# Performance work log

Measured on AMD Instinct MI355X. Metric: run time of the kernel, lower is better.

Reference implementation:

```python
import jax, jax.numpy as jnp
import numpy as np

EPS = 1e-06  # used both as eps and as the F.threshold threshold (mqjs passes eps as th)


def _pair_log_dist_sum(x1, x2, th):
    # dist[i,j] = ||x1_i||^2 + ||x2_j||^2 - 2 x1_i . x2_j  (n x n)
    x1x2 = x1 @ x2.T
    sq1 = jnp.sum(x1 * x1, axis=1)[:, None]
    sq2 = jnp.sum(x2 * x2, axis=1)[None, :]
    dist = sq1 + sq2 - 2.0 * x1x2
    # F.threshold(dist, th, 1): values <= th -> 1; then clamp(min=1), sqrt, log, row-sum
    dist = jnp.where(dist > th, dist, 1.0)
    dist = jnp.maximum(dist, 1.0)
    return jnp.sum(0.5 * jnp.log(dist), axis=1)  # log(sqrt(d)) == 0.5*log(d)


def _mqjs(inp, tgt, eps):
    n = inp.shape[0]
    x1 = inp.reshape(n, -1)
    x2 = tgt.reshape(n, -1)
    p = (x1 + x2) / 2.0
    ce = _pair_log_dist_sum(x1, p, eps) + _pair_log_dist_sum(x2, p, eps)
    se = _pair_log_dist_sum(x1, x1, eps) * (n / (n - 1))
    return jnp.mean(ce - se)


def setup_inputs() -> dict:
    key = jax.random.key(0)
    k1, k2 = jax.random.split(key)
    n, d = 8192, 256
    inp = jax.random.normal(k1, (n, d), dtype=jnp.float32)
    tgt = jax.random.normal(k2, (n, d), dtype=jnp.float32)
    return {"input": inp, "target": tgt}


def reference(input, target):
    return _mqjs(input, target, EPS)
```

## Files before the change

### kernel.cpp

```cpp
#include <hip/hip_runtime.h>

#define N 8192
#define D 256
#define BM 128
#define BJ 64
#define JG 8
#define GJ (N / BJ / JG)
#define GI (N / BM)

typedef int   i32x4 __attribute__((ext_vector_type(4)));
typedef int   i32x8 __attribute__((ext_vector_type(8)));
typedef float f32x4 __attribute__((ext_vector_type(4)));
typedef float f32x2 __attribute__((ext_vector_type(2)));

__device__ __forceinline__ unsigned pack_fp8x4(float a, float b, float c, float d) {
    unsigned lo = __builtin_amdgcn_cvt_pk_fp8_f32(a, b, 0, false);
    return __builtin_amdgcn_cvt_pk_fp8_f32(c, d, lo, true);
}
__device__ __forceinline__ float dequant_sumsq(unsigned q) {
    const float v0 = __builtin_amdgcn_cvt_f32_fp8(q, 0);
    const float v1 = __builtin_amdgcn_cvt_f32_fp8(q, 1);
    const float v2 = __builtin_amdgcn_cvt_f32_fp8(q, 2);
    const float v3 = __builtin_amdgcn_cvt_f32_fp8(q, 3);
    return fmaf(v0, v0, fmaf(v1, v1, fmaf(v2, v2, v3 * v3)));
}

__global__ void prep_kernel(const float* __restrict__ x1, const float* __restrict__ x2,
                            unsigned* __restrict__ x1q, unsigned* __restrict__ x2q,
                            unsigned* __restrict__ pq,
                            float* __restrict__ sq1, float* __restrict__ sq2,
                            float* __restrict__ sqp) {
    const int tid = threadIdx.x, lane = tid & 63, wv = tid >> 6;
    const int row = blockIdx.x * 4 + wv;
    const size_t eb = (size_t)row * D + lane * 4;
    const float4 a = *(const float4*)(x1 + eb);
    const float4 b = *(const float4*)(x2 + eb);
    const float px = 0.5f * (a.x + b.x), py = 0.5f * (a.y + b.y);
    const float pz = 0.5f * (a.z + b.z), pw = 0.5f * (a.w + b.w);
    const unsigned qa = pack_fp8x4(a.x, a.y, a.z, a.w);
    const unsigned qb = pack_fp8x4(b.x, b.y, b.z, b.w);
    const unsigned qp = pack_fp8x4(px, py, pz, pw);
    const size_t wb = (size_t)row * (D / 4) + lane;
    x1q[wb] = qa; x2q[wb] = qb; pq[wb] = qp;
    float s1 = dequant_sumsq(qa), s2 = dequant_sumsq(qb), sp = dequant_sumsq(qp);
    #pragma unroll
    for (int o = 32; o > 0; o >>= 1) {
        s1 += __shfl_down(s1, o, 64);
        s2 += __shfl_down(s2, o, 64);
        sp += __shfl_down(sp, o, 64);
    }
    if (lane == 0) { sq1[row] = s1; sq2[row] = s2; sqp[row] = sp; }
}

__device__ __forceinline__ f32x4 mfma8(i32x8 a, i32x8 b, f32x4 c) {
    return __builtin_amdgcn_mfma_scale_f32_16x16x128_f8f6f4(
        a, b, c, 0, 0, 0, 0x7F7F7F7F, 0, 0x7F7F7F7F);
}

__device__ __forceinline__ i32x8 read_frag(const unsigned char* Ts, int m, int quad) {
    const int r7 = m & 7;
    const i32x4 lo = *(const i32x4*)(Ts + m * 128 + ((((2 * quad)     ^ r7)) << 4));
    const i32x4 hi = *(const i32x4*)(Ts + m * 128 + ((((2 * quad + 1) ^ r7)) << 4));
    i32x8 f;
    f[0] = lo[0]; f[1] = lo[1]; f[2] = lo[2]; f[3] = lo[3];
    f[4] = hi[0]; f[5] = hi[1]; f[6] = hi[2]; f[7] = hi[3];
    return f;
}

__device__ __forceinline__ void stageA(const unsigned char* __restrict__ g,
                                       unsigned char* s, int rowbase, size_t kb,
                                       int wv, int srow, int sblk) {
    #pragma unroll
    for (int it = 0; it < 4; ++it) {
        const int grp = wv * 4 + it;
        const int row = grp * 8 + srow;
        __builtin_amdgcn_global_load_lds(
            (const __attribute__((address_space(1))) void*)(g + (size_t)(rowbase + row) * D + kb + sblk * 16),
            (__attribute__((address_space(3))) void*)(s + grp * 1024), 16, 0, 0);
    }
}
__device__ __forceinline__ void stageB(const unsigned char* __restrict__ g,
                                       unsigned char* s, int rowbase, size_t kb,
                                       int wv, int srow, int sblk) {
    #pragma unroll
    for (int it = 0; it < 2; ++it) {
        const int grp = wv * 2 + it;
        const int row = grp * 8 + srow;
        __builtin_amdgcn_global_load_lds(
            (const __attribute__((address_space(1))) void*)(g + (size_t)(rowbase + row) * D + kb + sblk * 16),
            (__attribute__((address_space(3))) void*)(s + grp * 1024), 16, 0, 0);
    }
}

__device__ __forceinline__ float logsumP(const f32x4 (&acc)[4][2],
                                         const float* __restrict__ sqA,
                                         const float sb[2], int wr, int quad) {
    float s = 0.0f;
    #pragma unroll
    for (int ti = 0; ti < 4; ++ti) {
        const int base = wr * 64 + ti * 16 + quad * 4;
        const f32x2 sa01 = {sqA[base], sqA[base + 1]};
        const f32x2 sa23 = {sqA[base + 2], sqA[base + 3]};
        f32x2 pr = {1.0f, 1.0f};
        #pragma unroll
        for (int tj = 0; tj < 2; ++tj) {
            const f32x2 sbv = {sb[tj], sb[tj]};
            const f32x2 t01 = sa01 + sbv, t23 = sa23 + sbv;
            const f32x2 v01 = {acc[ti][tj][0], acc[ti][tj][1]};
            const f32x2 v23 = {acc[ti][tj][2], acc[ti][tj][3]};
            f32x2 d01 = t01 - 2.0f * v01;
            f32x2 d23 = t23 - 2.0f * v23;
            d01 = __builtin_elementwise_max(d01, (f32x2){1.0f, 1.0f});
            d23 = __builtin_elementwise_max(d23, (f32x2){1.0f, 1.0f});
            pr *= d01; pr *= d23;
        }
        s += __logf(pr.x * pr.y);
    }
    return s;
}

__device__ __forceinline__ float logsumStraddle(const f32x4 (&acc)[4][2],
                                                const float* __restrict__ sqA,
                                                const float sb[2],
                                                int wr, int wc, int quad, int l15,
                                                int I0, int J0) {
    float s = 0.0f;
    #pragma unroll
    for (int ti = 0; ti < 4; ++ti) {
        #pragma unroll
        for (int tj = 0; tj < 2; ++tj) {
            const int j = J0 + wc * 32 + tj * 16 + l15;
            float pr = 1.0f;
            #pragma unroll
            for (int r = 0; r < 4; ++r) {
                const int i = I0 + wr * 64 + ti * 16 + quad * 4 + r;
                float d = fmaf(-2.0f, acc[ti][tj][r],
                               sqA[wr * 64 + ti * 16 + quad * 4 + r] + sb[tj]);
                d = fmaxf(d, 1.0f);
                const float t = (j > i) ? d : 1.0f;
                const float u = (j >= i) ? d : 1.0f;
                pr *= t * u;
            }
            s += __logf(pr);
        }
    }
    return s;
}

__global__ __launch_bounds__(256) void mqjs_main(
    const unsigned char* __restrict__ x1q, const unsigned char* __restrict__ x2q,
    const unsigned char* __restrict__ pq,
    const float* __restrict__ sq1, const float* __restrict__ sq2,
    const float* __restrict__ sqp, float* __restrict__ partials) {

    __shared__ __align__(16) unsigned char A2s[2 * BM * 128];
    __shared__ __align__(16) unsigned char BAs[2 * BJ * 128];
    __shared__ __align__(16) unsigned char BBs[2 * BJ * 128];
    __shared__ float sqa1[BM], sqa2[BM];
    __shared__ float red[4];

    const int tid = threadIdx.x;
    const int lane = tid & 63;
    const int wv = tid >> 6;
    const int wr = wv >> 1, wc = wv & 1;
    const int quad = lane >> 4, l15 = lane & 15;

    const int I0 = blockIdx.y * BM;
    const int jbase = blockIdx.x * JG;
    const float wse = -(float)N / (float)(N - 1);

    const int srow = lane >> 3;
    const int sblk = (lane & 7) ^ srow;

    stageA(x1q, A2s,         I0, 0,   wv, srow, sblk);
    stageA(x1q, A2s + 16384, I0, 128, wv, srow, sblk);
    stageB(pq,  BAs,         jbase * BJ, 0,   wv, srow, sblk);
    stageB(pq,  BAs + 8192,  jbase * BJ, 128, wv, srow, sblk);
    if (tid < BM) sqa1[tid] = sq1[I0 + tid];
    else          sqa2[tid - BM] = sq2[I0 + tid - BM];
    __syncthreads();

    i32x8 a1f[2][4];
    #pragma unroll
    for (int kc = 0; kc < 2; ++kc)
        #pragma unroll
        for (int ti = 0; ti < 4; ++ti)
            a1f[kc][ti] = read_frag(A2s + kc * 16384, wr * 64 + ti * 16 + l15, quad);
    __syncthreads();
    stageA(x2q, A2s,         I0, 0,   wv, srow, sblk);
    stageA(x2q, A2s + 16384, I0, 128, wv, srow, sblk);
    __syncthreads();

    float tsum = 0.0f;

    for (int jj = 0; jj < JG; ++jj) {
        const int J0 = (jbase + jj) * BJ;
        const bool doSym = (J0 >= I0);
        const bool full  = (J0 >= I0 + BM);

        f32x4 acc0[4][2], acc1[4][2];
        #pragma unroll
        for (int a = 0; a < 4; ++a)
            #pragma unroll
            for (int b = 0; b < 2; ++b) {
                acc0[a][b] = (f32x4){0.f, 0.f, 0.f, 0.f};
                acc1[a][b] = (f32x4){0.f, 0.f, 0.f, 0.f};
            }
        #pragma unroll
        for (int kc = 0; kc < 2; ++kc) {
            i32x8 bfr[2];
            #pragma unroll
            for (int tj = 0; tj < 2; ++tj)
                bfr[tj] = read_frag(BAs + kc * 8192, wc * 32 + tj * 16 + l15, quad);
            #pragma unroll
            for (int ti = 0; ti < 4; ++ti) {
                const i32x8 a2 = read_frag(A2s + kc * 16384, wr * 64 + ti * 16 + l15, quad);
                #pragma unroll
                for (int tj = 0; tj < 2; ++tj) {
                    acc0[ti][tj] = mfma8(a1f[kc][ti], bfr[tj], acc0[ti][tj]);
                    acc1[ti][tj] = mfma8(a2,          bfr[tj], acc1[ti][tj]);
                }
            }
        }

        if (doSym) {
            stageB(x1q, BBs,        J0, 0,   wv, srow, sblk);
            stageB(x1q, BBs + 8192, J0, 128, wv, srow, sblk);
        }

        {
            float sbp[2];
            #pragma unroll
            for (int tj = 0; tj < 2; ++tj) sbp[tj] = sqp[J0 + wc * 32 + tj * 16 + l15];
            tsum += 0.5f * logsumP(acc0, sqa1, sbp, wr, quad);
            tsum += 0.5f * logsumP(acc1, sqa2, sbp, wr, quad);
        }
        __syncthreads();

        f32x4 acc2[4][2];
        if (doSym) {
            #pragma unroll
            for (int a = 0; a < 4; ++a)
                #pragma unroll
                for (int b = 0; b < 2; ++b)
                    acc2[a][b] = (f32x4){0.f, 0.f, 0.f, 0.f};
            #pragma unroll
            for (int kc = 0; kc < 2; ++kc) {
                i32x8 bfr[2];
                #pragma unroll
                for (int tj = 0; tj < 2; ++tj)
                    bfr[tj] = read_frag(BBs + kc * 8192, wc * 32 + tj * 16 + l15, quad);
                #pragma unroll
                for (int ti = 0; ti < 4; ++ti)
                    #pragma unroll
                    for (int tj = 0; tj < 2; ++tj)
                        acc2[ti][tj] = mfma8(a1f[kc][ti], bfr[tj], acc2[ti][tj]);
            }
        }

        if (jj < JG - 1) {
            stageB(pq, BAs,        (jbase + jj + 1) * BJ, 0,   wv, srow, sblk);
            stageB(pq, BAs + 8192, (jbase + jj + 1) * BJ, 128, wv, srow, sblk);
        }

        if (doSym) {
            float sbx[2];
            #pragma unroll
            for (int tj = 0; tj < 2; ++tj) sbx[tj] = sq1[J0 + wc * 32 + tj * 16 + l15];
            if (full)
                tsum += wse * logsumP(acc2, sqa1, sbx, wr, quad);
            else
                tsum += 0.5f * wse * logsumStraddle(acc2, sqa1, sbx, wr, wc, quad, l15, I0, J0);
        }
        __syncthreads();
    }

    #pragma unroll
    for (int o = 32; o > 0; o >>= 1) tsum += __shfl_down(tsum, o, 64);
    if (lane == 0) red[wv] = tsum;
    __syncthreads();
    if (tid == 0)
        partials[blockIdx.y * GJ + blockIdx.x] = red[0] + red[1] + red[2] + red[3];
}

__global__ void finalize_kernel(const float* __restrict__ partials, float* __restrict__ out) {
    const int tid = threadIdx.x;
    const float4 v = ((const float4*)partials)[tid];
    double s = (double)v.x + (double)v.y + (double)v.z + (double)v.w;
    #pragma unroll
    for (int o = 32; o > 0; o >>= 1) s += __shfl_down(s, o, 64);
    __shared__ double r[4];
    if ((tid & 63) == 0) r[tid >> 6] = s;
    __syncthreads();
    if (tid == 0) out[0] = (float)((r[0] + r[1] + r[2] + r[3]) / (double)N);
}

extern "C" void kernel_launch(void* const* d_in, const int* in_sizes, int n_in,
                              void* d_out, int out_size, void* d_ws, size_t ws_size,
                              hipStream_t stream) {
    const float* x1 = (const float*)d_in[0];
    const float* x2 = (const float*)d_in[1];

    char* ws = (char*)d_ws;
    const size_t MBYTES = (size_t)N * D;
    unsigned* x1q = (unsigned*)(ws);
    unsigned* x2q = (unsigned*)(ws + MBYTES);
    unsigned* pq  = (unsigned*)(ws + 2 * MBYTES);
    float* sq1 = (float*)(ws + 3 * MBYTES);
    float* sq2 = (float*)(ws + 3 * MBYTES + (size_t)N * 4);
    float* sqp = (float*)(ws + 3 * MBYTES + (size_t)N * 8);
    float* partials = (float*)(ws + 3 * MBYTES + (size_t)N * 12);

    prep_kernel<<<N / 4, 256, 0, stream>>>(x1, x2, x1q, x2q, pq, sq1, sq2, sqp);
    mqjs_main<<<dim3(GJ, GI), 256, 0, stream>>>(
        (const unsigned char*)x1q, (const unsigned char*)x2q, (const unsigned char*)pq,
        sq1, sq2, sqp, partials);
    finalize_kernel<<<1, 256, 0, stream>>>(partials, (float*)d_out);
}
```

Measured before the change: 153.5 us.

## Merge B buffers, halve j-group, fuse finalize via atomic last-block reduction

Measured after the change: 186.4 us. 21.5% more time.

```diff
diff --git a/kernel.cpp b/kernel.cpp
--- a/kernel.cpp
+++ b/kernel.cpp
@@ -4,9 +4,10 @@
 #define D 256
 #define BM 128
 #define BJ 64
-#define JG 8
+#define JG 4
 #define GJ (N / BJ / JG)
 #define GI (N / BM)
+#define NBLK (GJ * GI)
 
 typedef int   i32x4 __attribute__((ext_vector_type(4)));
 typedef int   i32x8 __attribute__((ext_vector_type(8)));
@@ -29,9 +30,11 @@
                             unsigned* __restrict__ x1q, unsigned* __restrict__ x2q,
                             unsigned* __restrict__ pq,
                             float* __restrict__ sq1, float* __restrict__ sq2,
-                            float* __restrict__ sqp) {
+                            float* __restrict__ sqp, double* __restrict__ acc,
+                            unsigned* __restrict__ ctr) {
     const int tid = threadIdx.x, lane = tid & 63, wv = tid >> 6;
     const int row = blockIdx.x * 4 + wv;
+    if (blockIdx.x == 0 && tid == 0) { *acc = 0.0; *ctr = 0u; }
     const size_t eb = (size_t)row * D + lane * 4;
     const float4 a = *(const float4*)(x1 + eb);
     const float4 b = *(const float4*)(x2 + eb);
@@ -151,11 +154,11 @@
     const unsigned char* __restrict__ x1q, const unsigned char* __restrict__ x2q,
     const unsigned char* __restrict__ pq,
     const float* __restrict__ sq1, const float* __restrict__ sq2,
-    const float* __restrict__ sqp, float* __restrict__ partials) {
+    const float* __restrict__ sqp, double* __restrict__ acc_out,
+    unsigned* __restrict__ ctr, float* __restrict__ out) {
 
     __shared__ __align__(16) unsigned char A2s[2 * BM * 128];
-    __shared__ __align__(16) unsigned char BAs[2 * BJ * 128];
-    __shared__ __align__(16) unsigned char BBs[2 * BJ * 128];
+    __shared__ __align__(16) unsigned char Bs [2 * BJ * 128];
     __shared__ float sqa1[BM], sqa2[BM];
     __shared__ float red[4];
 
@@ -174,8 +177,8 @@
 
     stageA(x1q, A2s,         I0, 0,   wv, srow, sblk);
     stageA(x1q, A2s + 16384, I0, 128, wv, srow, sblk);
-    stageB(pq,  BAs,         jbase * BJ, 0,   wv, srow, sblk);
-    stageB(pq,  BAs + 8192,  jbase * BJ, 128, wv, srow, sblk);
+    stageB(pq,  Bs,          jbase * BJ, 0,   wv, srow, sblk);
+    stageB(pq,  Bs + 8192,   jbase * BJ, 128, wv, srow, sblk);
     if (tid < BM) sqa1[tid] = sq1[I0 + tid];
     else          sqa2[tid - BM] = sq2[I0 + tid - BM];
     __syncthreads();
@@ -198,7 +201,7 @@
         const bool doSym = (J0 >= I0);
         const bool full  = (J0 >= I0 + BM);
 
-        f32x4 acc0[4][2], acc1[4][2];
+        f32x4 acc0[4][2], acc1[4][2], acc2[4][2];
         #pragma unroll
         for (int a = 0; a < 4; ++a)
             #pragma unroll
@@ -211,7 +214,7 @@
             i32x8 bfr[2];
             #pragma unroll
             for (int tj = 0; tj < 2; ++tj)
-                bfr[tj] = read_frag(BAs + kc * 8192, wc * 32 + tj * 16 + l15, quad);
+                bfr[tj] = read_frag(Bs + kc * 8192, wc * 32 + tj * 16 + l15, quad);
             #pragma unroll
             for (int ti = 0; ti < 4; ++ti) {
                 const i32x8 a2 = read_frag(A2s + kc * 16384, wr * 64 + ti * 16 + l15, quad);
@@ -222,12 +225,12 @@
                 }
             }
         }
+        __syncthreads();
 
         if (doSym) {
-            stageB(x1q, BBs,        J0, 0,   wv, srow, sblk);
-            stageB(x1q, BBs + 8192, J0, 128, wv, srow, sblk);
-        }
-
+            stageB(x1q, Bs,        J0, 0,   wv, srow, sblk);
+            stageB(x1q, Bs + 8192, J0, 128, wv, srow, sblk);
+        }
         {
             float sbp[2];
             #pragma unroll
@@ -235,10 +238,9 @@
             tsum += 0.5f * logsumP(acc0, sqa1, sbp, wr, quad);
             tsum += 0.5f * logsumP(acc1, sqa2, sbp, wr, quad);
         }
-        __syncthreads();
-
-        f32x4 acc2[4][2];
+
         if (doSym) {
+            __syncthreads();
             #pragma unroll
             for (int a = 0; a < 4; ++a)
                 #pragma unroll
@@ -249,20 +251,20 @@
                 i32x8 bfr[2];
                 #pragma unroll
                 for (int tj = 0; tj < 2; ++tj)
-                    bfr[tj] = read_frag(BBs + kc * 8192, wc * 32 + tj * 16 + l15, quad);
+                    bfr[tj] = read_frag(Bs + kc * 8192, wc * 32 + tj * 16 + l15, quad);
                 #pragma unroll
                 for (int ti = 0; ti < 4; ++ti)
                     #pragma unroll
                     for (int tj = 0; tj < 2; ++tj)
                         acc2[ti][tj] = mfma8(a1f[kc][ti], bfr[tj], acc2[ti][tj]);
             }
+            __syncthreads();
         }
 
         if (jj < JG - 1) {
-            stageB(pq, BAs,        (jbase + jj + 1) * BJ, 0,   wv, srow, sblk);
-            stageB(pq, BAs + 8192, (jbase + jj + 1) * BJ, 128, wv, srow, sblk);
-        }
-
+            stageB(pq, Bs,        (jbase + jj + 1) * BJ, 0,   wv, srow, sblk);
+            stageB(pq, Bs + 8192, (jbase + jj + 1) * BJ, 128, wv, srow, sblk);
+        }
         if (doSym) {
             float sbx[2];
             #pragma unroll
@@ -279,20 +281,16 @@
     for (int o = 32; o > 0; o >>= 1) tsum += __shfl_down(tsum, o, 64);
     if (lane == 0) red[wv] = tsum;
     __syncthreads();
-    if (tid == 0)
-        partials[blockIdx.y * GJ + blockIdx.x] = red[0] + red[1] + red[2] + red[3];
-}
-
-__global__ void finalize_kernel(const float* __restrict__ partials, float* __restrict__ out) {
-    const int tid = threadIdx.x;
-    const float4 v = ((const float4*)partials)[tid];
-    double s = (double)v.x + (double)v.y + (double)v.z + (double)v.w;
-    #pragma unroll
-    for (int o = 32; o > 0; o >>= 1) s += __shfl_down(s, o, 64);
-    __shared__ double r[4];
-    if ((tid & 63) == 0) r[tid >> 6] = s;
-    __syncthreads();
-    if (tid == 0) out[0] = (float)((r[0] + r[1] + r[2] + r[3]) / (double)N);
+    if (tid == 0) {
+        atomicAdd(acc_out, (double)(red[0] + red[1] + red[2] + red[3]));
+        __threadfence();
+        const unsigned prev = atomicAdd(ctr, 1u);
+        if (prev == NBLK - 1) {
+            __threadfence();
+            const double tot = atomicAdd(acc_out, 0.0);
+            out[0] = (float)(tot / (double)N);
+        }
+    }
 }
 
 extern "C" void kernel_launch(void* const* d_in, const int* in_sizes, int n_in,
@@ -309,11 +307,11 @@
     float* sq1 = (float*)(ws + 3 * MBYTES);
     float* sq2 = (float*)(ws + 3 * MBYTES + (size_t)N * 4);
     float* sqp = (float*)(ws + 3 * MBYTES + (size_t)N * 8);
-    float* partials = (float*)(ws + 3 * MBYTES + (size_t)N * 12);
-
-    prep_kernel<<<N / 4, 256, 0, stream>>>(x1, x2, x1q, x2q, pq, sq1, sq2, sqp);
+    double* acc = (double*)(ws + 3 * MBYTES + (size_t)N * 12);
+    unsigned* ctr = (unsigned*)(ws + 3 * MBYTES + (size_t)N * 12 + 16);
+
+    prep_kernel<<<N / 4, 256, 0, stream>>>(x1, x2, x1q, x2q, pq, sq1, sq2, sqp, acc, ctr);
     mqjs_main<<<dim3(GJ, GI), 256, 0, stream>>>(
         (const unsigned char*)x1q, (const unsigned char*)x2q, (const unsigned char*)pq,
-        sq1, sq2, sqp, partials);
-    finalize_kernel<<<1, 256, 0, stream>>>(partials, (float*)d_out);
-}
+        sq1, sq2, sqp, acc, ctr, (float*)d_out);
+}
```

## Load A-side fp8 fragments directly into registers and overlap B prefetch with epilogue

Applied to the files above, without the earlier changes.

Result: slower. 166.3 us (+8.4%).

```diff
diff --git a/kernel.cpp b/kernel.cpp
--- a/kernel.cpp
+++ b/kernel.cpp
@@ -67,18 +67,6 @@
     return f;
 }
 
-__device__ __forceinline__ void stageA(const unsigned char* __restrict__ g,
-                                       unsigned char* s, int rowbase, size_t kb,
-                                       int wv, int srow, int sblk) {
-    #pragma unroll
-    for (int it = 0; it < 4; ++it) {
-        const int grp = wv * 4 + it;
-        const int row = grp * 8 + srow;
-        __builtin_amdgcn_global_load_lds(
-            (const __attribute__((address_space(1))) void*)(g + (size_t)(rowbase + row) * D + kb + sblk * 16),
-            (__attribute__((address_space(3))) void*)(s + grp * 1024), 16, 0, 0);
-    }
-}
 __device__ __forceinline__ void stageB(const unsigned char* __restrict__ g,
                                        unsigned char* s, int rowbase, size_t kb,
                                        int wv, int srow, int sblk) {
@@ -153,7 +141,6 @@
     const float* __restrict__ sq1, const float* __restrict__ sq2,
     const float* __restrict__ sqp, float* __restrict__ partials) {
 
-    __shared__ __align__(16) unsigned char A2s[2 * BM * 128];
     __shared__ __align__(16) unsigned char BAs[2 * BJ * 128];
     __shared__ __align__(16) unsigned char BBs[2 * BJ * 128];
     __shared__ float sqa1[BM], sqa2[BM];
@@ -172,23 +159,20 @@
     const int srow = lane >> 3;
     const int sblk = (lane & 7) ^ srow;
 
-    stageA(x1q, A2s,         I0, 0,   wv, srow, sblk);
-    stageA(x1q, A2s + 16384, I0, 128, wv, srow, sblk);
-    stageB(pq,  BAs,         jbase * BJ, 0,   wv, srow, sblk);
-    stageB(pq,  BAs + 8192,  jbase * BJ, 128, wv, srow, sblk);
+    stageB(pq, BAs,        jbase * BJ, 0,   wv, srow, sblk);
+    stageB(pq, BAs + 8192, jbase * BJ, 128, wv, srow, sblk);
     if (tid < BM) sqa1[tid] = sq1[I0 + tid];
     else          sqa2[tid - BM] = sq2[I0 + tid - BM];
-    __syncthreads();
-
-    i32x8 a1f[2][4];
+
+    i32x8 a1f[2][4], a2f[2][4];
     #pragma unroll
     for (int kc = 0; kc < 2; ++kc)
         #pragma unroll
-        for (int ti = 0; ti < 4; ++ti)
-            a1f[kc][ti] = read_frag(A2s + kc * 16384, wr * 64 + ti * 16 + l15, quad);
-    __syncthreads();
-    stageA(x2q, A2s,         I0, 0,   wv, srow, sblk);
-    stageA(x2q, A2s + 16384, I0, 128, wv, srow, sblk);
+        for (int ti = 0; ti < 4; ++ti) {
+            const size_t ro = (size_t)(I0 + wr * 64 + ti * 16 + l15) * D + kc * 128 + quad * 32;
+            a1f[kc][ti] = *(const i32x8*)(x1q + ro);
+            a2f[kc][ti] = *(const i32x8*)(x2q + ro);
+        }
     __syncthreads();
 
     float tsum = 0.0f;
@@ -213,32 +197,26 @@
             for (int tj = 0; tj < 2; ++tj)
                 bfr[tj] = read_frag(BAs + kc * 8192, wc * 32 + tj * 16 + l15, quad);
             #pragma unroll
-            for (int ti = 0; ti < 4; ++ti) {
-                const i32x8 a2 = read_frag(A2s + kc * 16384, wr * 64 + ti * 16 + l15, quad);
+            for (int ti = 0; ti < 4; ++ti)
                 #pragma unroll
                 for (int tj = 0; tj < 2; ++tj) {
                     acc0[ti][tj] = mfma8(a1f[kc][ti], bfr[tj], acc0[ti][tj]);
-                    acc1[ti][tj] = mfma8(a2,          bfr[tj], acc1[ti][tj]);
+                    acc1[ti][tj] = mfma8(a2f[kc][ti], bfr[tj], acc1[ti][tj]);
                 }
-            }
-        }
+        }
+
+        float sbp[2];
+        #pragma unroll
+        for (int tj = 0; tj < 2; ++tj) sbp[tj] = sqp[J0 + wc * 32 + tj * 16 + l15];
 
         if (doSym) {
             stageB(x1q, BBs,        J0, 0,   wv, srow, sblk);
             stageB(x1q, BBs + 8192, J0, 128, wv, srow, sblk);
-        }
-
-        {
-            float sbp[2];
-            #pragma unroll
-            for (int tj = 0; tj < 2; ++tj) sbp[tj] = sqp[J0 + wc * 32 + tj * 16 + l15];
             tsum += 0.5f * logsumP(acc0, sqa1, sbp, wr, quad);
             tsum += 0.5f * logsumP(acc1, sqa2, sbp, wr, quad);
-        }
-        __syncthreads();
-
-        f32x4 acc2[4][2];
-        if (doSym) {
+            __syncthreads();
+
+            f32x4 acc2[4][2];
             #pragma unroll
             for (int a = 0; a < 4; ++a)
                 #pragma unroll
@@ -256,14 +234,10 @@
                     for (int tj = 0; tj < 2; ++tj)
                         acc2[ti][tj] = mfma8(a1f[kc][ti], bfr[tj], acc2[ti][tj]);
             }
-        }
-
-        if (jj < JG - 1) {
-            stageB(pq, BAs,        (jbase + jj + 1) * BJ, 0,   wv, srow, sblk);
-            stageB(pq, BAs + 8192, (jbase + jj + 1) * BJ, 128, wv, srow, sblk);
-        }
-
-        if (doSym) {
+            if (jj < JG - 1) {
+                stageB(pq, BAs,        (jbase + jj + 1) * BJ, 0,   wv, srow, sblk);
+                stageB(pq, BAs + 8192, (jbase + jj + 1) * BJ, 128, wv, srow, sblk);
+            }
             float sbx[2];
             #pragma unroll
             for (int tj = 0; tj < 2; ++tj) sbx[tj] = sq1[J0 + wc * 32 + tj * 16 + l15];
@@ -271,8 +245,17 @@
                 tsum += wse * logsumP(acc2, sqa1, sbx, wr, quad);
             else
                 tsum += 0.5f * wse * logsumStraddle(acc2, sqa1, sbx, wr, wc, quad, l15, I0, J0);
-        }
-        __syncthreads();
+            __syncthreads();
+        } else {
+            __syncthreads();
+            if (jj < JG - 1) {
+                stageB(pq, BAs,        (jbase + jj + 1) * BJ, 0,   wv, srow, sblk);
+                stageB(pq, BAs + 8192, (jbase + jj + 1) * BJ, 128, wv, srow, sblk);
+            }
+            tsum += 0.5f * logsumP(acc0, sqa1, sbp, wr, quad);
+            tsum += 0.5f * logsumP(acc1, sqa2, sbp, wr, quad);
+            __syncthreads();
+        }
     }
 
     #pragma unroll
```
